# Kernel tuning notes

Measured on AMD Instinct MI355X. Metric: run time of the kernel, lower is better.

## Reference

```python
import jax, jax.numpy as jnp
import numpy as np

FORMULA_OH_SIZES = [20, 20, 20, 20, 20]
SPECT_BIN_N = 512


def layer_norm(x, g, b, eps=1e-5):
    m = jnp.mean(x, axis=-1, keepdims=True)
    v = jnp.var(x, axis=-1, keepdims=True)
    return (x - m) * jax.lax.rsqrt(v + eps) * g + b


def gru_cell(x, h, W_ih, W_hh, b_ih, b_hh):
    # torch.nn.GRUCell math
    gi = x @ W_ih.T + b_ih
    gh = h @ W_hh.T + b_hh
    i_r, i_z, i_n = jnp.split(gi, 3, axis=-1)
    h_r, h_z, h_n = jnp.split(gh, 3, axis=-1)
    r = jax.nn.sigmoid(i_r + h_r)
    z = jax.nn.sigmoid(i_z + h_z)
    n = jnp.tanh(i_n + r * h_n)
    return (1.0 - z) * n + z * h


def structured_one_hot(x, sizes, accum=True):
    # x: [N, len(sizes)] integer element counts -> concatenated (accumulated) one-hots
    outs = []
    for i, s in enumerate(sizes):
        v = jnp.clip(x[:, i].astype(jnp.int32), 0, s - 1)
        if accum:
            oh = (jnp.arange(s)[None, :] <= v[:, None]).astype(jnp.float32)  # thermometer
        else:
            oh = jax.nn.one_hot(v, s, dtype=jnp.float32)
        outs.append(oh)
    return jnp.concatenate(outs, axis=-1)


def setup_inputs():
    key = jax.random.key(0)
    ks = jax.random.split(key, 16)
    B, A, GF, HW, S, M = 16, 32, 128, 4, 4096, 8
    G = GF * HW                       # 512 = g_feat_in * highway_steps_n
    FE = sum(FORMULA_OH_SIZES)        # 100
    D = 512                           # internal_d
    vert_feat_in = jax.random.normal(ks[0], (B, A, GF, HW), jnp.float32)
    vert_mask_in = jnp.ones((B, A), jnp.float32)
    elem_id = jax.random.randint(ks[1], (B, A), 0, 5)
    vert_element_oh = jax.nn.one_hot(elem_id, 5, dtype=jnp.float32)
    adj_oh = jnp.zeros((B, A, A, 4), jnp.float32)  # unused by forward
    atom_subsets = jax.random.bernoulli(ks[2], 0.5, (B, S, A)).astype(jnp.float32)
    masses = jax.random.uniform(ks[3], (B, S, M), jnp.float32, 0.0, SPECT_BIN_N - 1.0)
    intens = jax.random.uniform(ks[4], (B, S, M), jnp.float32)
    atom_subsets_peaks = jnp.stack([masses, intens], axis=-1)

    def lin(k, o, i):
        return (jax.random.normal(k, (o, i), jnp.float32) / np.sqrt(i)).astype(jnp.float32)

    return dict(
        vert_feat_in=vert_feat_in, vert_mask_in=vert_mask_in,
        vert_element_oh=vert_element_oh, adj_oh=adj_oh,
        atom_subsets=atom_subsets, atom_subsets_peaks=atom_subsets_peaks,
        ln_sub_g=jnp.ones((G,), jnp.float32), ln_sub_b=jnp.zeros((G,), jnp.float32),
        W_ih=lin(ks[5], 3 * G, FE), W_hh=lin(ks[6], 3 * G, G),
        b_ih=jnp.zeros((3 * G,), jnp.float32), b_hh=jnp.zeros((3 * G,), jnp.float32),
        W1=lin(ks[7], D, G), b1=jnp.zeros((D,), jnp.float32),
        W2a=lin(ks[8], D, D), b2a=jnp.zeros((D,), jnp.float32),
        W2b=lin(ks[9], D, D), b2b=jnp.zeros((D,), jnp.float32),
        ln_pre_g=jnp.ones((D,), jnp.float32), ln_pre_b=jnp.zeros((D,), jnp.float32),
        Ws=lin(ks[10], 1, D), bs=jnp.zeros((1,), jnp.float32),
    )


def reference(vert_feat_in, vert_mask_in, vert_element_oh, adj_oh, atom_subsets,
              atom_subsets_peaks, ln_sub_g, ln_sub_b, W_ih, W_hh, b_ih, b_hh,
              W1, b1, W2a, b2a, W2b, b2b, ln_pre_g, ln_pre_b, Ws, bs):
    B, A, GF, HW = vert_feat_in.shape
    S = atom_subsets.shape[1]
    vf = vert_feat_in.reshape(B, A, GF * HW)                       # [B,A,G]
    masked_vf = vf * vert_mask_in[:, :, None]
    subs_m = atom_subsets * vert_mask_in[:, None, :]               # [B,S,A]
    swvs = jnp.einsum('bag,bsa->bsg', masked_vf, subs_m)           # [B,S,G]
    # per-subset element counts -> structured one-hot formula encoding
    counts = jnp.einsum('bae,bsa->bse', vert_element_oh, atom_subsets).astype(jnp.int32)
    pf_flat = structured_one_hot(counts.reshape(B * S, -1), FORMULA_OH_SIZES, accum=True)
    subset_size = jnp.sum(subs_m, axis=2) + 1e-4                   # [B,S]
    mean = swvs / subset_size[:, :, None]
    normed = layer_norm(mean, ln_sub_g, ln_sub_b)                  # [B,S,G]
    h = gru_cell(pf_flat, normed.reshape(B * S, -1), W_ih, W_hh, b_ih, b_hh)
    h = h.reshape(normed.shape)
    x = jax.nn.relu(h @ W1.T + b1)
    x = jax.nn.relu(x @ W2a.T + b2a)
    x = jax.nn.relu(x @ W2b.T + b2b)   # (extra F.relu in original is idempotent)
    x = layer_norm(x, ln_pre_g, ln_pre_b)
    scores = (x @ Ws.T + bs)[..., 0]                               # [B,S]
    probs = jax.nn.softmax(scores, axis=-1)
    # mass histogram: scatter intensity*prob into rounded-mass bins
    masses = atom_subsets_peaks[..., 0]                            # [B,S,M]
    intens = atom_subsets_peaks[..., 1]
    bins = jnp.clip(jnp.round(masses).astype(jnp.int32), 0, SPECT_BIN_N - 1)
    contrib = intens * probs[:, :, None]                           # [B,S,M]
    spect = jnp.zeros((B, SPECT_BIN_N), x.dtype).at[
        jnp.arange(B)[:, None], bins.reshape(B, -1)].add(contrib.reshape(B, -1))
    return (spect, probs)
```

## Files before the change

kernel.cpp:

```cpp
#include <hip/hip_runtime.h>
#include <math.h>

#define B_ 16
#define A_ 32
#define G_ 512
#define S_ 4096
#define M_ 8
#define BS_ 65536
#define KC_ 640
#define NG_ 1536

typedef _Float16 half8 __attribute__((ext_vector_type(8)));
typedef _Float16 half4v __attribute__((ext_vector_type(4)));
typedef _Float16 half2v __attribute__((ext_vector_type(2)));
typedef float floatx4 __attribute__((ext_vector_type(4)));

typedef const __attribute__((address_space(1))) void* gas_t;
typedef __attribute__((address_space(3))) void* las_t;

__device__ __forceinline__ float wave_sum_f(float v){
#pragma unroll
  for (int o = 32; o > 0; o >>= 1) v += __shfl_xor(v, o);
  return v;
}
__device__ __forceinline__ float wave_max_f(float v){
#pragma unroll
  for (int o = 32; o > 0; o >>= 1) v = fmaxf(v, __shfl_xor(v, o));
  return v;
}
__device__ __forceinline__ float sigmoidf_(float x){ return 1.f/(1.f+__expf(-x)); }
__device__ __forceinline__ float tanhf_(float x){ return 1.f - 2.f/(__expf(2.f*x)+1.f); }

__global__ __launch_bounds__(256) void k_cvt3(const float* __restrict__ s0,
                                              const float* __restrict__ s1,
                                              const float* __restrict__ s2,
                                              _Float16* __restrict__ d){
  const float* s = (blockIdx.y == 0) ? s0 : (blockIdx.y == 1) ? s1 : s2;
  int i = (blockIdx.x*256 + threadIdx.x)*4;
  if (i >= G_*G_) return;
  float4 v = *(const float4*)(s+i);
  half4v o; o[0]=(_Float16)v.x; o[1]=(_Float16)v.y; o[2]=(_Float16)v.z; o[3]=(_Float16)v.w;
  *(half4v*)(d + (size_t)blockIdx.y*G_*G_ + i) = o;
}

__global__ __launch_bounds__(64) void k_buildw(const float* __restrict__ Whh,
                                               const float* __restrict__ Wih,
                                               _Float16* __restrict__ Wcat){
  int j = blockIdx.x;
  for (int p = threadIdx.x; p < KC_; p += 64){
    float v = 0.f;
    if (p < 512) v = Whh[(size_t)j*512 + p];
    else if (p < 612) v = Wih[(size_t)j*100 + (p - 512)];
    Wcat[(size_t)j*KC_ + p] = (_Float16)v;
  }
}

__global__ __launch_bounds__(256) void k_prep_mfma(
    const float* __restrict__ vf, const float* __restrict__ mask,
    const float* __restrict__ eoh, const float* __restrict__ subs,
    const float* __restrict__ ln_g, const float* __restrict__ ln_b,
    _Float16* __restrict__ Abuf){
  __shared__ _Float16 s_mvfT[G_*A_];
  __shared__ _Float16 s_sm[128*A_];
  __shared__ float s_m[A_];
  __shared__ float s_e[A_*5];
  __shared__ float s_ssum[128];
  __shared__ float s_red1[2][4][16];
  __shared__ float s_red2[2][4][16];
  int tid = threadIdx.x;
  int bx = blockIdx.x, b = blockIdx.y;
  int lane = tid & 63, w = tid >> 6;
  int q = lane >> 4, l15 = lane & 15;
  size_t row0 = (size_t)b*S_ + (size_t)bx*128;
  if (tid < A_)   s_m[tid] = mask[b*A_ + tid];
  if (tid < A_*5) s_e[tid] = eoh[b*A_*5 + tid];
  __syncthreads();
  {
    int p = tid & 15, gseg = tid >> 4;
    float mk0 = s_m[2*p], mk1 = s_m[2*p+1];
    const float* v0 = vf + ((size_t)b*A_ + 2*p)*G_ + gseg*32;
    const float* v1 = v0 + G_;
#pragma unroll
    for (int i = 0; i < 32; i += 4){
      float4 a = *(const float4*)(v0 + i);
      float4 c = *(const float4*)(v1 + i);
      float av[4] = {a.x, a.y, a.z, a.w};
      float cv[4] = {c.x, c.y, c.z, c.w};
#pragma unroll
      for (int j = 0; j < 4; ++j){
        half2v h; h[0] = (_Float16)(av[j]*mk0); h[1] = (_Float16)(cv[j]*mk1);
        *(half2v*)(s_mvfT + (gseg*32 + i + j)*A_ + 2*p) = h;
      }
    }
  }
  {
    int s = tid >> 1, hh = tid & 1;
    const float* sp = subs + (row0 + s)*A_ + hh*16;
    _Float16* dst = s_sm + s*A_ + hh*16;
#pragma unroll
    for (int i = 0; i < 16; i += 4){
      float4 v = *(const float4*)(sp + i);
      half4v h; h[0]=(_Float16)v.x; h[1]=(_Float16)v.y; h[2]=(_Float16)v.z; h[3]=(_Float16)v.w;
      *(half4v*)(dst + i) = h;
    }
  }
  __syncthreads();
  if (tid < 128){
    int s = tid;
    float ssum = 0.f, c0=0.f, c1=0.f, c2=0.f, c3=0.f, c4=0.f;
#pragma unroll
    for (int a = 0; a < A_; ++a){
      float v = (float)s_sm[s*A_ + a];
      ssum += v * s_m[a];
      c0 += v * s_e[a*5+0]; c1 += v * s_e[a*5+1]; c2 += v * s_e[a*5+2];
      c3 += v * s_e[a*5+3]; c4 += v * s_e[a*5+4];
    }
    int cc[5];
    cc[0] = min(max((int)(c0+0.5f),0),19); cc[1] = min(max((int)(c1+0.5f),0),19);
    cc[2] = min(max((int)(c2+0.5f),0),19); cc[3] = min(max((int)(c3+0.5f),0),19);
    cc[4] = min(max((int)(c4+0.5f),0),19);
    s_ssum[s] = ssum;
    _Float16* dst = Abuf + (row0 + s)*KC_ + 512;
#pragma unroll
    for (int t = 0; t < 16; ++t){
      half8 hv;
#pragma unroll
      for (int u = 0; u < 8; ++u){
        int k = t*8 + u;
        float v = 0.f;
        if (k < 100){ int f = k/20, l = k - f*20; v = (l <= cc[f]) ? 1.f : 0.f; }
        hv[u] = (_Float16)v;
      }
      *(half8*)(dst + t*8) = hv;
    }
  }
  half8 bf[8]; float lng[8], lnb[8];
#pragma unroll
  for (int t = 0; t < 8; ++t){
    int g = w*128 + t*16 + l15;
    bf[t] = *(const half8*)(s_mvfT + g*A_ + q*8);
    lng[t] = ln_g[g]; lnb[t] = ln_b[g];
  }
  __syncthreads();
  for (int gi = 0; gi < 8; ++gi){
    half8 af = *(const half8*)(s_sm + (gi*16 + l15)*A_ + q*8);
    floatx4 c[8];
#pragma unroll
    for (int t = 0; t < 8; ++t){
      floatx4 z = {0.f, 0.f, 0.f, 0.f};
      c[t] = __builtin_amdgcn_mfma_f32_16x16x32_f16(af, bf[t], z, 0, 0, 0);
    }
    float p1[4] = {0.f,0.f,0.f,0.f}, p2[4] = {0.f,0.f,0.f,0.f};
#pragma unroll
    for (int t = 0; t < 8; ++t)
#pragma unroll
      for (int r = 0; r < 4; ++r){ float v = c[t][r]; p1[r] += v; p2[r] += v*v; }
#pragma unroll
    for (int off = 1; off < 16; off <<= 1)
#pragma unroll
      for (int r = 0; r < 4; ++r){
        p1[r] += __shfl_xor(p1[r], off);
        p2[r] += __shfl_xor(p2[r], off);
      }
    int gb = gi & 1;
    if (l15 == 0){
#pragma unroll
      for (int r = 0; r < 4; ++r){ s_red1[gb][w][q*4+r] = p1[r]; s_red2[gb][w][q*4+r] = p2[r]; }
    }
    __syncthreads();
#pragma unroll
    for (int r = 0; r < 4; ++r){
      int sl = gi*16 + q*4 + r;
      int rr = q*4 + r;
      float t1 = s_red1[gb][0][rr] + s_red1[gb][1][rr] + s_red1[gb][2][rr] + s_red1[gb][3][rr];
      float t2 = s_red2[gb][0][rr] + s_red2[gb][1][rr] + s_red2[gb][2][rr] + s_red2[gb][3][rr];
      float inv = 1.f/(s_ssum[sl] + 1e-4f);
      float mu = t1*inv*(1.f/512.f);
      float var = t2*inv*inv*(1.f/512.f) - mu*mu;
      float rs = rsqrtf(var + 1e-5f);
      _Float16* orow = Abuf + (row0 + sl)*KC_;
#pragma unroll
      for (int t = 0; t < 8; ++t){
        float o = (c[t][r]*inv - mu)*rs*lng[t] + lnb[t];
        orow[w*128 + t*16 + l15] = (_Float16)o;
      }
    }
  }
}

__global__ __launch_bounds__(512) void k_gru_fused(
    const _Float16* __restrict__ Abuf, const _Float16* __restrict__ Wcat,
    const float* __restrict__ bih, const float* __restrict__ bhh,
    _Float16* __restrict__ H){
  __shared__ _Float16 smA[128*32];
  __shared__ _Float16 smB[192*32];
  int tid = threadIdx.x;
  int lane = tid & 63, wvid = tid >> 6;
  int wm = wvid & 1, wn = wvid >> 1;
  int q = lane >> 4, l15 = lane & 15;
  int mt = blockIdx.x*64 + (blockIdx.y >> 3);
  int dt = blockIdx.y & 7;
  int m0 = mt*128, n0 = dt*64;
  floatx4 acc[3][4] = {};
  floatx4 accNI[4] = {};
  int offA[4], offB[3];
#pragma unroll
  for (int i = 0; i < 4; ++i){
    int r = wm*64 + i*16 + l15;
    offA[i] = (r*4 + (q ^ ((r>>2)&3)))*8;
  }
#pragma unroll
  for (int g = 0; g < 3; ++g){
    int rb = g*64 + wn*16 + l15;
    offB[g] = (rb*4 + (q ^ ((rb>>2)&3)))*8;
  }
  const _Float16* gA;
  {
    int u = wvid*64 + lane;
    int r = u >> 2, c = (u & 3) ^ ((r >> 2) & 3);
    gA = Abuf + (size_t)(m0 + r)*KC_ + c*8;
  }
  const _Float16* gB0;
  {
    int u = wvid*64 + lane;
    int rb = u >> 2, c = (u & 3) ^ ((rb >> 2) & 3);
    int grow = (rb >> 6)*512 + n0 + (rb & 63);
    gB0 = Wcat + (size_t)grow*KC_ + c*8;
  }
  const _Float16* gB1 = nullptr;
  if (wvid < 4){
    int u = (8 + wvid)*64 + lane;
    int rb = u >> 2, c = (u & 3) ^ ((rb >> 2) & 3);
    int grow = (rb >> 6)*512 + n0 + (rb & 63);
    gB1 = Wcat + (size_t)grow*KC_ + c*8;
  }
  for (int kc = 0; kc < 512; kc += 32){
    __builtin_amdgcn_global_load_lds((gas_t)(gA + kc), (las_t)(smA + wvid*512), 16, 0, 0);
    __builtin_amdgcn_global_load_lds((gas_t)(gB0 + kc), (las_t)(smB + wvid*512), 16, 0, 0);
    if (wvid < 4)
      __builtin_amdgcn_global_load_lds((gas_t)(gB1 + kc), (las_t)(smB + (8+wvid)*512), 16, 0, 0);
    __syncthreads();
    half8 af[4], bfv[3];
#pragma unroll
    for (int i = 0; i < 4; ++i) af[i] = *(const half8*)(smA + offA[i]);
#pragma unroll
    for (int g = 0; g < 3; ++g) bfv[g] = *(const half8*)(smB + offB[g]);
#pragma unroll
    for (int g = 0; g < 3; ++g)
#pragma unroll
      for (int i = 0; i < 4; ++i)
        acc[g][i] = __builtin_amdgcn_mfma_f32_16x16x32_f16(af[i], bfv[g], acc[g][i], 0, 0, 0);
    __syncthreads();
  }
  for (int kc = 512; kc < KC_; kc += 32){
    __builtin_amdgcn_global_load_lds((gas_t)(gA + kc), (las_t)(smA + wvid*512), 16, 0, 0);
    __builtin_amdgcn_global_load_lds((gas_t)(gB0 + kc), (las_t)(smB + wvid*512), 16, 0, 0);
    if (wvid < 4)
      __builtin_amdgcn_global_load_lds((gas_t)(gB1 + kc), (las_t)(smB + (8+wvid)*512), 16, 0, 0);
    __syncthreads();
    half8 af[4], bfv[3];
#pragma unroll
    for (int i = 0; i < 4; ++i) af[i] = *(const half8*)(smA + offA[i]);
#pragma unroll
    for (int g = 0; g < 3; ++g) bfv[g] = *(const half8*)(smB + offB[g]);
#pragma unroll
    for (int i = 0; i < 4; ++i){
      acc[0][i] = __builtin_amdgcn_mfma_f32_16x16x32_f16(af[i], bfv[0], acc[0][i], 0, 0, 0);
      acc[1][i] = __builtin_amdgcn_mfma_f32_16x16x32_f16(af[i], bfv[1], acc[1][i], 0, 0, 0);
      accNI[i]  = __builtin_amdgcn_mfma_f32_16x16x32_f16(af[i], bfv[2], accNI[i], 0, 0, 0);
    }
    __syncthreads();
  }
  int d = n0 + wn*16 + l15;
  float br  = bih[d] + bhh[d];
  float bz  = bih[512+d] + bhh[512+d];
  float bnh = bhh[1024+d];
  float bni = bih[1024+d];
#pragma unroll
  for (int i = 0; i < 4; ++i){
#pragma unroll
    for (int r = 0; r < 4; ++r){
      int m = m0 + wm*64 + i*16 + q*4 + r;
      float gr  = acc[0][i][r] + br;
      float gz  = acc[1][i][r] + bz;
      float hn  = acc[2][i][r] + bnh;
      float in_ = accNI[i][r] + bni;
      float rrv = sigmoidf_(gr);
      float zz  = sigmoidf_(gz);
      float nn  = tanhf_(in_ + rrv*hn);
      float hp  = (float)Abuf[(size_t)m*KC_ + d];
      H[(size_t)m*G_ + d] = (_Float16)((1.f-zz)*nn + zz*hp);
    }
  }
}

__global__ __launch_bounds__(256) void k_gemm(
    const _Float16* __restrict__ A, const _Float16* __restrict__ W,
    const float* __restrict__ bias, _Float16* __restrict__ Out){
  __shared__ _Float16 smA[128*32];
  __shared__ _Float16 smB[128*32];
  int tid = threadIdx.x;
  int lane = tid & 63, wvid = tid >> 6;
  int wm = wvid & 1, wn = wvid >> 1;
  int q = lane >> 4, l15 = lane & 15;
  int mt = blockIdx.x*64 + (blockIdx.y >> 2);
  int nt = blockIdx.y & 3;
  int m0 = mt*128, n0 = nt*128;
  floatx4 acc[4][4] = {};
  int offA[4], offB[4];
#pragma unroll
  for (int i = 0; i < 4; ++i){
    int r = wm*64 + i*16 + l15;
    offA[i] = (r*4 + (q ^ ((r>>2)&3)))*8;
    int rb = wn*64 + i*16 + l15;
    offB[i] = (rb*4 + (q ^ ((rb>>2)&3)))*8;
  }
  int uA[2];
  const _Float16 *gA[2], *gB[2];
#pragma unroll
  for (int t = 0; t < 2; ++t){
    int seg = wvid*2 + t;
    int u = seg*64 + lane;
    int r = u >> 2, c = (u & 3) ^ ((r >> 2) & 3);
    uA[t] = seg;
    gA[t] = A + (size_t)(m0 + r)*G_ + c*8;
    gB[t] = W + (size_t)(n0 + r)*G_ + c*8;
  }
  for (int kc = 0; kc < G_; kc += 32){
#pragma unroll
    for (int t = 0; t < 2; ++t){
      __builtin_amdgcn_global_load_lds((gas_t)(gA[t] + kc), (las_t)(smA + uA[t]*512), 16, 0, 0);
      __builtin_amdgcn_global_load_lds((gas_t)(gB[t] + kc), (las_t)(smB + uA[t]*512), 16, 0, 0);
    }
    __syncthreads();
    half8 af[4], bfv[4];
#pragma unroll
    for (int i = 0; i < 4; ++i) af[i] = *(const half8*)(smA + offA[i]);
#pragma unroll
    for (int j = 0; j < 4; ++j) bfv[j] = *(const half8*)(smB + offB[j]);
#pragma unroll
    for (int i = 0; i < 4; ++i)
#pragma unroll
      for (int j = 0; j < 4; ++j)
        acc[i][j] = __builtin_amdgcn_mfma_f32_16x16x32_f16(af[i], bfv[j], acc[i][j], 0, 0, 0);
    __syncthreads();
  }
#pragma unroll
  for (int j = 0; j < 4; ++j){
    int n = n0 + wn*64 + j*16 + l15;
    float bv = bias[n];
#pragma unroll
    for (int i = 0; i < 4; ++i){
#pragma unroll
      for (int r = 0; r < 4; ++r){
        int m = m0 + wm*64 + i*16 + q*4 + r;
        Out[(size_t)m*G_ + n] = (_Float16)fmaxf(acc[i][j][r] + bv, 0.f);
      }
    }
  }
}

__global__ __launch_bounds__(256) void k_ff3_fin(
    const _Float16* __restrict__ A, const _Float16* __restrict__ W,
    const float* __restrict__ bias, const float* __restrict__ ln_pre_g,
    const float* __restrict__ Ws, float* __restrict__ Pbuf){
  __shared__ _Float16 smA[128*32];
  __shared__ _Float16 smB[128*32];
  __shared__ float sP[2][64][2][3];
  int tid = threadIdx.x;
  int lane = tid & 63, wvid = tid >> 6;
  int wm = wvid & 1, wn = wvid >> 1;
  int q = lane >> 4, l15 = lane & 15;
  int mt = blockIdx.x*64 + (blockIdx.y >> 2);
  int nt = blockIdx.y & 3;
  int m0 = mt*128, n0 = nt*128;
  floatx4 acc[4][4] = {};
  int offA[4], offB[4];
#pragma unroll
  for (int i = 0; i < 4; ++i){
    int r = wm*64 + i*16 + l15;
    offA[i] = (r*4 + (q ^ ((r>>2)&3)))*8;
    int rb = wn*64 + i*16 + l15;
    offB[i] = (rb*4 + (q ^ ((rb>>2)&3)))*8;
  }
  int uA[2];
  const _Float16 *gA[2], *gB[2];
#pragma unroll
  for (int t = 0; t < 2; ++t){
    int seg = wvid*2 + t;
    int u = seg*64 + lane;
    int r = u >> 2, c = (u & 3) ^ ((r >> 2) & 3);
    uA[t] = seg;
    gA[t] = A + (size_t)(m0 + r)*G_ + c*8;
    gB[t] = W + (size_t)(n0 + r)*G_ + c*8;
  }
  for (int kc = 0; kc < G_; kc += 32){
#pragma unroll
    for (int t = 0; t < 2; ++t){
      __builtin_amdgcn_global_load_lds((gas_t)(gA[t] + kc), (las_t)(smA + uA[t]*512), 16, 0, 0);
      __builtin_amdgcn_global_load_lds((gas_t)(gB[t] + kc), (las_t)(smB + uA[t]*512), 16, 0, 0);
    }
    __syncthreads();
    half8 af[4], bfv[4];
#pragma unroll
    for (int i = 0; i < 4; ++i) af[i] = *(const half8*)(smA + offA[i]);
#pragma unroll
    for (int j = 0; j < 4; ++j) bfv[j] = *(const half8*)(smB + offB[j]);
#pragma unroll
    for (int i = 0; i < 4; ++i)
#pragma unroll
      for (int j = 0; j < 4; ++j)
        acc[i][j] = __builtin_amdgcn_mfma_f32_16x16x32_f16(af[i], bfv[j], acc[i][j], 0, 0, 0);
    __syncthreads();
  }
  float gws[4], bv4[4];
#pragma unroll
  for (int j = 0; j < 4; ++j){
    int n = n0 + wn*64 + j*16 + l15;
    gws[j] = ln_pre_g[n]*Ws[n];
    bv4[j] = bias[n];
  }
#pragma unroll
  for (int i = 0; i < 4; ++i){
#pragma unroll
    for (int r = 0; r < 4; ++r){
      float p1 = 0.f, p2 = 0.f, p3 = 0.f;
#pragma unroll
      for (int j = 0; j < 4; ++j){
        float x = fmaxf(acc[i][j][r] + bv4[j], 0.f);
        p1 += x; p2 += x*x; p3 += gws[j]*x;
      }
#pragma unroll
      for (int off = 1; off < 16; off <<= 1){
        p1 += __shfl_xor(p1, off);
        p2 += __shfl_xor(p2, off);
        p3 += __shfl_xor(p3, off);
      }
      if (l15 == 0){
        int rl = i*16 + q*4 + r;
        sP[wm][rl][wn][0] = p1; sP[wm][rl][wn][1] = p2; sP[wm][rl][wn][2] = p3;
      }
    }
  }
  __syncthreads();
  if (tid < 128){
    int wmi = tid >> 6, rl = tid & 63;
    int m = m0 + wmi*64 + rl;
    float* dst = Pbuf + ((size_t)m*4 + nt)*3;
    dst[0] = sP[wmi][rl][0][0] + sP[wmi][rl][1][0];
    dst[1] = sP[wmi][rl][0][1] + sP[wmi][rl][1][1];
    dst[2] = sP[wmi][rl][0][2] + sP[wmi][rl][1][2];
  }
}

__global__ __launch_bounds__(256) void k_score_fin(
    const float* __restrict__ Pbuf, const float* __restrict__ g,
    const float* __restrict__ bta, const float* __restrict__ Ws,
    const float* __restrict__ bs, float* __restrict__ scores){
  __shared__ float red[8];
  int tid = threadIdx.x, lane = tid & 63, wv = tid >> 6;
  int i0 = tid*2;
  float c1p = g[i0]*Ws[i0] + g[i0+1]*Ws[i0+1];
  float c2p = bta[i0]*Ws[i0] + bta[i0+1]*Ws[i0+1];
  c1p = wave_sum_f(c1p); c2p = wave_sum_f(c2p);
  if (lane == 0){ red[wv] = c1p; red[4+wv] = c2p; }
  __syncthreads();
  float c1 = red[0]+red[1]+red[2]+red[3];
  float c2 = red[4]+red[5]+red[6]+red[7] + bs[0];
  size_t row = (size_t)blockIdx.x*256 + tid;
  const float* p = Pbuf + row*12;
  float4 a  = *(const float4*)p;
  float4 b4 = *(const float4*)(p+4);
  float4 c4 = *(const float4*)(p+8);
  float P1 = a.x + a.w + b4.z + c4.y;
  float P2 = a.y + b4.x + b4.w + c4.z;
  float P3 = a.z + b4.y + c4.x + c4.w;
  float mu = P1*(1.f/512.f);
  float var = P2*(1.f/512.f) - mu*mu;
  float rs = rsqrtf(var + 1e-5f);
  scores[row] = rs*(P3 - mu*c1) + c2;
}

__global__ __launch_bounds__(256) void k_softmax(
    const float* __restrict__ scores, float* __restrict__ probs){
  __shared__ float red[4];
  int b = blockIdx.x, tid = threadIdx.x, lane = tid & 63, wv = tid >> 6;
  const float* sp = scores + (size_t)b*S_;
  float mx = -1e30f;
  for (int i = tid; i < S_; i += 256) mx = fmaxf(mx, sp[i]);
  mx = wave_max_f(mx);
  if (lane == 0) red[wv] = mx;
  __syncthreads();
  mx = fmaxf(fmaxf(red[0], red[1]), fmaxf(red[2], red[3]));
  __syncthreads();
  float sum = 0.f;
  for (int i = tid; i < S_; i += 256) sum += __expf(sp[i]-mx);
  sum = wave_sum_f(sum);
  if (lane == 0) red[wv] = sum;
  __syncthreads();
  sum = red[0]+red[1]+red[2]+red[3];
  float inv = 1.f/sum;
  for (int i = tid; i < S_; i += 256)
    probs[(size_t)b*S_ + i] = __expf(sp[i]-mx)*inv;
}

__global__ __launch_bounds__(256) void k_spect(
    const float* __restrict__ peaks, const float* __restrict__ probs,
    float* __restrict__ spect){
  __shared__ float bins[512];
  int b = blockIdx.x, tid = threadIdx.x;
  bins[tid] = 0.f; bins[tid+256] = 0.f;
  __syncthreads();
  for (int i = tid; i < S_*M_; i += 256){
    int s = i >> 3, m = i & 7;
    const float* pk = peaks + (((size_t)b*S_ + s)*M_ + m)*2;
    float mass = pk[0], inten = pk[1];
    float p = probs[(size_t)b*S_ + s];
    int bin = (int)rintf(mass);
    bin = min(max(bin, 0), 511);
    atomicAdd(&bins[bin], inten*p);
  }
  __syncthreads();
  spect[(size_t)b*512 + tid]       = bins[tid];
  spect[(size_t)b*512 + tid + 256] = bins[tid+256];
}

extern "C" void kernel_launch(void* const* d_in, const int* in_sizes, int n_in,
                              void* d_out, int out_size, void* d_ws, size_t ws_size,
                              hipStream_t stream) {
  const float* vf       = (const float*)d_in[0];
  const float* mask     = (const float*)d_in[1];
  const float* eoh      = (const float*)d_in[2];
  const float* subs     = (const float*)d_in[4];
  const float* peaks    = (const float*)d_in[5];
  const float* ln_sub_g = (const float*)d_in[6];
  const float* ln_sub_b = (const float*)d_in[7];
  const float* W_ih     = (const float*)d_in[8];
  const float* W_hh     = (const float*)d_in[9];
  const float* b_ih     = (const float*)d_in[10];
  const float* b_hh     = (const float*)d_in[11];
  const float* W1       = (const float*)d_in[12];
  const float* b1       = (const float*)d_in[13];
  const float* W2a      = (const float*)d_in[14];
  const float* b2a      = (const float*)d_in[15];
  const float* W2b      = (const float*)d_in[16];
  const float* b2b      = (const float*)d_in[17];
  const float* ln_pre_g = (const float*)d_in[18];
  const float* ln_pre_b = (const float*)d_in[19];
  const float* Ws       = (const float*)d_in[20];
  const float* bs       = (const float*)d_in[21];
  float* out = (float*)d_out;
  float* probs_out = out + (size_t)B_*512;

  char* w = (char*)d_ws;
  float* scores = (float*)w;     w += (size_t)BS_*4;
  float* Pbuf   = (float*)w;     w += (size_t)BS_*12*4;
  _Float16* Wcat = (_Float16*)w; w += (size_t)NG_*KC_*2;
  _Float16* W1h  = (_Float16*)w; w += (size_t)G_*G_*2;
  _Float16* W2ah = (_Float16*)w; w += (size_t)G_*G_*2;
  _Float16* W2bh = (_Float16*)w; w += (size_t)G_*G_*2;
  _Float16* Abuf = (_Float16*)w; w += (size_t)BS_*KC_*2;
  _Float16* bufh0 = (_Float16*)w;
  _Float16* bufh1 = Abuf;

  k_cvt3<<<dim3((G_*G_/4+255)/256, 3), 256, 0, stream>>>(W1, W2a, W2b, W1h);
  k_buildw<<<NG_, 64, 0, stream>>>(W_hh, W_ih, Wcat);
  k_prep_mfma<<<dim3(S_/128, B_), 256, 0, stream>>>(vf, mask, eoh, subs,
                                                    ln_sub_g, ln_sub_b, Abuf);
  k_gru_fused<<<dim3(8, 512), 512, 0, stream>>>(Abuf, Wcat, b_ih, b_hh, bufh0);
  k_gemm<<<dim3(8, 256), 256, 0, stream>>>(bufh0, W1h,  b1,  bufh1);
  k_gemm<<<dim3(8, 256), 256, 0, stream>>>(bufh1, W2ah, b2a, bufh0);
  k_ff3_fin<<<dim3(8, 256), 256, 0, stream>>>(bufh0, W2bh, b2b,
                                              ln_pre_g, Ws, Pbuf);
  k_score_fin<<<BS_/256, 256, 0, stream>>>(Pbuf, ln_pre_g, ln_pre_b, Ws, bs, scores);
  k_softmax<<<B_, 256, 0, stream>>>(scores, probs_out);
  k_spect<<<B_, 256, 0, stream>>>(peaks, probs_out, out);
}
```

Before: 557.0 us.

## Double-buffer LDS tiles in GRU and FF GEMM kernels to overlap loads

Converts the GRU fused kernel and the two feed-forward GEMM kernels from single-buffered LDS staging to ping-pong double buffering. The next K-chunk is fetched with global_load_lds while MFMAs run on the current chunk, and each iteration ends with one vmcnt wait plus a barrier instead of two __syncthreads. This is meant to hide global-memory latency behind compute, at the cost of doubled LDS use, which may lower occupancy. There is a possible hazard: LDS reads of the current buffer rely on the compiler waiting for lgkmcnt before the barrier, since the next iteration overwrites the other buffer.

```diff
diff --git a/kernel.cpp b/kernel.cpp
--- a/kernel.cpp
+++ b/kernel.cpp
@@ -192,8 +192,8 @@
     const _Float16* __restrict__ Abuf, const _Float16* __restrict__ Wcat,
     const float* __restrict__ bih, const float* __restrict__ bhh,
     _Float16* __restrict__ H){
-  __shared__ _Float16 smA[128*32];
-  __shared__ _Float16 smB[192*32];
+  __shared__ _Float16 smA[2][128*32];
+  __shared__ _Float16 smB[2][192*32];
   int tid = threadIdx.x;
   int lane = tid & 63, wvid = tid >> 6;
   int wm = wvid & 1, wn = wvid >> 1;
@@ -234,42 +234,43 @@
     int grow = (rb >> 6)*512 + n0 + (rb & 63);
     gB1 = Wcat + (size_t)grow*KC_ + c*8;
   }
-  for (int kc = 0; kc < 512; kc += 32){
-    __builtin_amdgcn_global_load_lds((gas_t)(gA + kc), (las_t)(smA + wvid*512), 16, 0, 0);
-    __builtin_amdgcn_global_load_lds((gas_t)(gB0 + kc), (las_t)(smB + wvid*512), 16, 0, 0);
-    if (wvid < 4)
-      __builtin_amdgcn_global_load_lds((gas_t)(gB1 + kc), (las_t)(smB + (8+wvid)*512), 16, 0, 0);
-    __syncthreads();
+  __builtin_amdgcn_global_load_lds((gas_t)gA,  (las_t)(smA[0] + wvid*512), 16, 0, 0);
+  __builtin_amdgcn_global_load_lds((gas_t)gB0, (las_t)(smB[0] + wvid*512), 16, 0, 0);
+  if (wvid < 4)
+    __builtin_amdgcn_global_load_lds((gas_t)gB1, (las_t)(smB[0] + (8+wvid)*512), 16, 0, 0);
+  asm volatile("s_waitcnt vmcnt(0)");
+  __builtin_amdgcn_s_barrier();
+  const int NT = KC_/32;
+  for (int t = 0; t < NT; ++t){
+    int cur = t & 1;
+    if (t + 1 < NT){
+      int kc = (t+1)*32;
+      __builtin_amdgcn_global_load_lds((gas_t)(gA + kc),  (las_t)(smA[cur^1] + wvid*512), 16, 0, 0);
+      __builtin_amdgcn_global_load_lds((gas_t)(gB0 + kc), (las_t)(smB[cur^1] + wvid*512), 16, 0, 0);
+      if (wvid < 4)
+        __builtin_amdgcn_global_load_lds((gas_t)(gB1 + kc), (las_t)(smB[cur^1] + (8+wvid)*512), 16, 0, 0);
+    }
     half8 af[4], bfv[3];
 #pragma unroll
-    for (int i = 0; i < 4; ++i) af[i] = *(const half8*)(smA + offA[i]);
-#pragma unroll
-    for (int g = 0; g < 3; ++g) bfv[g] = *(const half8*)(smB + offB[g]);
-#pragma unroll
-    for (int g = 0; g < 3; ++g)
-#pragma unroll
-      for (int i = 0; i < 4; ++i)
-        acc[g][i] = __builtin_amdgcn_mfma_f32_16x16x32_f16(af[i], bfv[g], acc[g][i], 0, 0, 0);
-    __syncthreads();
-  }
-  for (int kc = 512; kc < KC_; kc += 32){
-    __builtin_amdgcn_global_load_lds((gas_t)(gA + kc), (las_t)(smA + wvid*512), 16, 0, 0);
-    __builtin_amdgcn_global_load_lds((gas_t)(gB0 + kc), (las_t)(smB + wvid*512), 16, 0, 0);
-    if (wvid < 4)
-      __builtin_amdgcn_global_load_lds((gas_t)(gB1 + kc), (las_t)(smB + (8+wvid)*512), 16, 0, 0);
-    __syncthreads();
-    half8 af[4], bfv[3];
-#pragma unroll
-    for (int i = 0; i < 4; ++i) af[i] = *(const half8*)(smA + offA[i]);
-#pragma unroll
-    for (int g = 0; g < 3; ++g) bfv[g] = *(const half8*)(smB + offB[g]);
-#pragma unroll
-    for (int i = 0; i < 4; ++i){
-      acc[0][i] = __builtin_amdgcn_mfma_f32_16x16x32_f16(af[i], bfv[0], acc[0][i], 0, 0, 0);
-      acc[1][i] = __builtin_amdgcn_mfma_f32_16x16x32_f16(af[i], bfv[1], acc[1][i], 0, 0, 0);
-      accNI[i]  = __builtin_amdgcn_mfma_f32_16x16x32_f16(af[i], bfv[2], accNI[i], 0, 0, 0);
-    }
-    __syncthreads();
+    for (int i = 0; i < 4; ++i) af[i] = *(const half8*)(smA[cur] + offA[i]);
+#pragma unroll
+    for (int g = 0; g < 3; ++g) bfv[g] = *(const half8*)(smB[cur] + offB[g]);
+    if (t < 16){
+#pragma unroll
+      for (int g = 0; g < 3; ++g)
+#pragma unroll
+        for (int i = 0; i < 4; ++i)
+          acc[g][i] = __builtin_amdgcn_mfma_f32_16x16x32_f16(af[i], bfv[g], acc[g][i], 0, 0, 0);
+    } else {
+#pragma unroll
+      for (int i = 0; i < 4; ++i){
+        acc[0][i] = __builtin_amdgcn_mfma_f32_16x16x32_f16(af[i], bfv[0], acc[0][i], 0, 0, 0);
+        acc[1][i] = __builtin_amdgcn_mfma_f32_16x16x32_f16(af[i], bfv[1], acc[1][i], 0, 0, 0);
+        accNI[i]  = __builtin_amdgcn_mfma_f32_16x16x32_f16(af[i], bfv[2], accNI[i], 0, 0, 0);
+      }
+    }
+    asm volatile("s_waitcnt vmcnt(0)");
+    __builtin_amdgcn_s_barrier();
   }
   int d = n0 + wn*16 + l15;
   float br  = bih[d] + bhh[d];
@@ -297,8 +298,8 @@
 __global__ __launch_bounds__(256) void k_gemm(
     const _Float16* __restrict__ A, const _Float16* __restrict__ W,
     const float* __restrict__ bias, _Float16* __restrict__ Out){
-  __shared__ _Float16 smA[128*32];
-  __shared__ _Float16 smB[128*32];
+  __shared__ _Float16 smA[2][128*32];
+  __shared__ _Float16 smB[2][128*32];
   int tid = threadIdx.x;
   int lane = tid & 63, wvid = tid >> 6;
   int wm = wvid & 1, wn = wvid >> 1;
@@ -326,24 +327,36 @@
     gA[t] = A + (size_t)(m0 + r)*G_ + c*8;
     gB[t] = W + (size_t)(n0 + r)*G_ + c*8;
   }
-  for (int kc = 0; kc < G_; kc += 32){
-#pragma unroll
-    for (int t = 0; t < 2; ++t){
-      __builtin_amdgcn_global_load_lds((gas_t)(gA[t] + kc), (las_t)(smA + uA[t]*512), 16, 0, 0);
-      __builtin_amdgcn_global_load_lds((gas_t)(gB[t] + kc), (las_t)(smB + uA[t]*512), 16, 0, 0);
-    }
-    __syncthreads();
+#pragma unroll
+  for (int t2 = 0; t2 < 2; ++t2){
+    __builtin_amdgcn_global_load_lds((gas_t)(gA[t2]), (las_t)(smA[0] + uA[t2]*512), 16, 0, 0);
+    __builtin_amdgcn_global_load_lds((gas_t)(gB[t2]), (las_t)(smB[0] + uA[t2]*512), 16, 0, 0);
+  }
+  asm volatile("s_waitcnt vmcnt(0)");
+  __builtin_amdgcn_s_barrier();
+  const int NT = G_/32;
+  for (int t = 0; t < NT; ++t){
+    int cur = t & 1;
+    if (t + 1 < NT){
+      int kc = (t+1)*32;
+#pragma unroll
+      for (int t2 = 0; t2 < 2; ++t2){
+        __builtin_amdgcn_global_load_lds((gas_t)(gA[t2] + kc), (las_t)(smA[cur^1] + uA[t2]*512), 16, 0, 0);
+        __builtin_amdgcn_global_load_lds((gas_t)(gB[t2] + kc), (las_t)(smB[cur^1] + uA[t2]*512), 16, 0, 0);
+      }
+    }
     half8 af[4], bfv[4];
 #pragma unroll
-    for (int i = 0; i < 4; ++i) af[i] = *(const half8*)(smA + offA[i]);
-#pragma unroll
-    for (int j = 0; j < 4; ++j) bfv[j] = *(const half8*)(smB + offB[j]);
+    for (int i = 0; i < 4; ++i) af[i] = *(const half8*)(smA[cur] + offA[i]);
+#pragma unroll
+    for (int j = 0; j < 4; ++j) bfv[j] = *(const half8*)(smB[cur] + offB[j]);
 #pragma unroll
     for (int i = 0; i < 4; ++i)
 #pragma unroll
       for (int j = 0; j < 4; ++j)
         acc[i][j] = __builtin_amdgcn_mfma_f32_16x16x32_f16(af[i], bfv[j], acc[i][j], 0, 0, 0);
-    __syncthreads();
+    asm volatile("s_waitcnt vmcnt(0)");
+    __builtin_amdgcn_s_barrier();
   }
 #pragma unroll
   for (int j = 0; j < 4; ++j){
@@ -364,8 +377,8 @@
     const _Float16* __restrict__ A, const _Float16* __restrict__ W,
     const float* __restrict__ bias, const float* __restrict__ ln_pre_g,
     const float* __restrict__ Ws, float* __restrict__ Pbuf){
-  __shared__ _Float16 smA[128*32];
-  __shared__ _Float16 smB[128*32];
+  __shared__ _Float16 smA[2][128*32];
+  __shared__ _Float16 smB[2][128*32];
   __shared__ float sP[2][64][2][3];
   int tid = threadIdx.x;
   int lane = tid & 63, wvid = tid >> 6;
@@ -394,24 +407,36 @@
     gA[t] = A + (size_t)(m0 + r)*G_ + c*8;
     gB[t] = W + (size_t)(n0 + r)*G_ + c*8;
   }
-  for (int kc = 0; kc < G_; kc += 32){
-#pragma unroll
-    for (int t = 0; t < 2; ++t){
-      __builtin_amdgcn_global_load_lds((gas_t)(gA[t] + kc), (las_t)(smA + uA[t]*512), 16, 0, 0);
-      __builtin_amdgcn_global_load_lds((gas_t)(gB[t] + kc), (las_t)(smB + uA[t]*512), 16, 0, 0);
-    }
-    __syncthreads();
+#pragma unroll
+  for (int t2 = 0; t2 < 2; ++t2){
+    __builtin_amdgcn_global_load_lds((gas_t)(gA[t2]), (las_t)(smA[0] + uA[t2]*512), 16, 0, 0);
+    __builtin_amdgcn_global_load_lds((gas_t)(gB[t2]), (las_t)(smB[0] + uA[t2]*512), 16, 0, 0);
+  }
+  asm volatile("s_waitcnt vmcnt(0)");
+  __builtin_amdgcn_s_barrier();
+  const int NT = G_/32;
+  for (int t = 0; t < NT; ++t){
+    int cur = t & 1;
+    if (t + 1 < NT){
+      int kc = (t+1)*32;
+#pragma unroll
+      for (int t2 = 0; t2 < 2; ++t2){
+        __builtin_amdgcn_global_load_lds((gas_t)(gA[t2] + kc), (las_t)(smA[cur^1] + uA[t2]*512), 16, 0, 0);
+        __builtin_amdgcn_global_load_lds((gas_t)(gB[t2] + kc), (las_t)(smB[cur^1] + uA[t2]*512), 16, 0, 0);
+      }
+    }
     half8 af[4], bfv[4];
 #pragma unroll
-    for (int i = 0; i < 4; ++i) af[i] = *(const half8*)(smA + offA[i]);
-#pragma unroll
-    for (int j = 0; j < 4; ++j) bfv[j] = *(const half8*)(smB + offB[j]);
+    for (int i = 0; i < 4; ++i) af[i] = *(const half8*)(smA[cur] + offA[i]);
+#pragma unroll
+    for (int j = 0; j < 4; ++j) bfv[j] = *(const half8*)(smB[cur] + offB[j]);
 #pragma unroll
     for (int i = 0; i < 4; ++i)
 #pragma unroll
       for (int j = 0; j < 4; ++j)
         acc[i][j] = __builtin_amdgcn_mfma_f32_16x16x32_f16(af[i], bfv[j], acc[i][j], 0, 0, 0);
-    __syncthreads();
+    asm volatile("s_waitcnt vmcnt(0)");
+    __builtin_amdgcn_s_barrier();
   }
   float gws[4], bv4[4];
 #pragma unroll
```

New measurement: 525.8 us. 1.06x faster.
